# Kernel optimization log

Measured on AMD Instinct MI355X. Metric: run time of the kernel, lower is better.

Reference implementation:

```python
import jax, jax.numpy as jnp
import numpy as np

D = 1024      # model_dim
H = 2048      # expert hidden_dim
E = 8         # num routed experts
TOP_K = 2
N_SHARED = 1
B, S = 2, 1024


def setup_inputs() -> dict:
    key = jax.random.key(0)
    ks = jax.random.split(key, 12)
    sc = 0.02
    return {
        "hidden": jax.random.normal(ks[0], (B, S, D), jnp.float32),
        # router Linear(D -> E); stored as [in, out]
        "router_w": jax.random.normal(ks[1], (D, E), jnp.float32) * sc,
        "router_b": jnp.zeros((E,), jnp.float32),
        # shared expert (1): Linear(D->H), Linear(H->D)
        "sw1": jax.random.normal(ks[2], (D, H), jnp.float32) * sc,
        "sb1": jnp.zeros((H,), jnp.float32),
        "sw2": jax.random.normal(ks[3], (H, D), jnp.float32) * sc,
        "sb2": jnp.zeros((D,), jnp.float32),
        # routed experts, stacked over E
        "rw1": jax.random.normal(ks[4], (E, D, H), jnp.float32) * sc,
        "rb1": jnp.zeros((E, H), jnp.float32),
        "rw2": jax.random.normal(ks[5], (E, H, D), jnp.float32) * sc,
        "rb2": jnp.zeros((E, D), jnp.float32),
    }


def reference(hidden, router_w, router_b, sw1, sb1, sw2, sb2, rw1, rb1, rw2, rb2):
    b, s, d = hidden.shape
    T = b * s
    flat = hidden.reshape(T, d)                              # [T, D]

    # --- router ---
    router_logits = flat @ router_w + router_b               # [T, E]
    router_probs = jax.nn.softmax(router_logits, axis=-1)
    topk_probs, topk_idx = jax.lax.top_k(router_probs, TOP_K)  # [T, K]

    # per-(token, expert) mixing weight: sum of top-k probs that hit expert e
    weights = jnp.zeros_like(router_probs).at[
        jnp.arange(T)[:, None], topk_idx
    ].add(topk_probs)                                        # [T, E]

    # --- shared expert(s) (1 expert -> mean == itself) ---
    sh = jax.nn.gelu(flat @ sw1 + sb1, approximate=False)    # [T, H]
    shared_out = (sh @ sw2 + sb2) / N_SHARED                 # [T, D]

    # --- routed experts: dense all-expert eval weighted by routing weights ---
    # (identical math to the gather/FFN/index_add loop: weight is 0 for
    #  tokens not routed to expert e)
    h1 = jax.nn.gelu(jnp.einsum('td,edh->teh', flat, rw1) + rb1[None],
                     approximate=False)                      # [T, E, H]
    expert_out = jnp.einsum('teh,ehd->ted', h1, rw2) + rb2[None]  # [T, E, D]
    mixed = jnp.einsum('ted,te->td', expert_out, weights)    # [T, D]

    return (shared_out + mixed).reshape(b, s, d)
```

## Files before the change

### kernel.cpp

```cpp
#include <hip/hip_runtime.h>
#include <hip/hip_bf16.h>

#define T_TOK 2048
#define DDIM  1024
#define HDIM  2048
#define NEXP  8
#define NSEG  9

typedef unsigned short u16;
typedef __attribute__((ext_vector_type(4))) float f32x4;
typedef __attribute__((ext_vector_type(8))) short bf16x8;
typedef __attribute__((ext_vector_type(4))) unsigned short u16x4;

__device__ __forceinline__ u16 f2bf(float x) {
  union { float f; unsigned int u; } v; v.f = x;
  unsigned int r = v.u + 0x7fffu + ((v.u >> 16) & 1u);
  return (u16)(r >> 16);
}
__device__ __forceinline__ float gelu_exact(float x) {
  return 0.5f * x * (1.0f + erff(x * 0.70710678118654752f));
}

__device__ __forceinline__ void gload16(const void* g, void* l) {
  __builtin_amdgcn_global_load_lds(
      (const __attribute__((address_space(1))) unsigned int*)g,
      (__attribute__((address_space(3))) unsigned int*)l, 16, 0, 0);
}

__global__ __launch_bounds__(256) void router_kernel(
    const float* __restrict__ x, const float* __restrict__ rw,
    const float* __restrict__ rb, u16* __restrict__ xb,
    float* __restrict__ weights, int* __restrict__ counts,
    int* __restrict__ lists)
{
  int wv = threadIdx.x >> 6, lane = threadIdx.x & 63;
  int t = blockIdx.x * 4 + wv;
  const float* xrow = x + (size_t)t * DDIM;
  float acc[NEXP];
#pragma unroll
  for (int e = 0; e < NEXP; e++) acc[e] = 0.f;
#pragma unroll
  for (int i = 0; i < 4; i++) {
    int d0 = i * 256 + lane * 4;
    f32x4 xv = *(const f32x4*)(xrow + d0);
    u16x4 pk;
#pragma unroll
    for (int j = 0; j < 4; j++) {
      float xs = xv[j];
      pk[j] = f2bf(xs);
      const float* wr = rw + (size_t)(d0 + j) * NEXP;
#pragma unroll
      for (int e = 0; e < NEXP; e++) acc[e] = fmaf(xs, wr[e], acc[e]);
    }
    *(u16x4*)(xb + (size_t)t * DDIM + d0) = pk;
  }
#pragma unroll
  for (int off = 32; off >= 1; off >>= 1)
#pragma unroll
    for (int e = 0; e < NEXP; e++) acc[e] += __shfl_xor(acc[e], off);

  if (lane == 0) {
    float lg[NEXP], mx = -1e30f;
#pragma unroll
    for (int e = 0; e < NEXP; e++) { lg[e] = acc[e] + rb[e]; mx = fmaxf(mx, lg[e]); }
    float p[NEXP], s = 0.f;
#pragma unroll
    for (int e = 0; e < NEXP; e++) { p[e] = expf(lg[e] - mx); s += p[e]; }
    float inv = 1.0f / s;
#pragma unroll
    for (int e = 0; e < NEXP; e++) p[e] *= inv;
    int i1 = 0;
#pragma unroll
    for (int e = 1; e < NEXP; e++) if (p[e] > p[i1]) i1 = e;
    int i2 = (i1 == 0) ? 1 : 0;
#pragma unroll
    for (int e = 0; e < NEXP; e++) if (e != i1 && p[e] > p[i2]) i2 = e;
#pragma unroll
    for (int e = 0; e < NEXP; e++)
      weights[(size_t)t * NEXP + e] = (e == i1) ? p[i1] : (e == i2) ? p[i2] : 0.f;
    int p1 = atomicAdd(counts + i1, 1); lists[i1 * T_TOK + p1] = t;
    int p2 = atomicAdd(counts + i2, 1); lists[i2 * T_TOK + p2] = t;
    lists[NEXP * T_TOK + t] = t;
  }
}

__global__ void seg_kernel(int* counts, int* segoff, int* ytab, int* nyt) {
  counts[NEXP] = T_TOK;
  int off = 0, n = 0;
  for (int e = 0; e < NSEG; e++) {
    segoff[e] = off;
    int c = counts[e];
    for (int my = 0; my * 128 < c; my++) ytab[n++] = e * 256 + my;
    off += c;
  }
  *nyt = n;
}

__global__ __launch_bounds__(256) void transpose_bf16_kernel(
    const float* __restrict__ rin, const float* __restrict__ sin_,
    u16* __restrict__ rout, u16* __restrict__ sout, int R, int C)
{
  __shared__ float tile[32][33];
  int b = blockIdx.z;
  const float* inb = (b < NEXP) ? rin + (size_t)b * R * C : sin_;
  u16* outb = (b < NEXP) ? rout + (size_t)b * R * C : sout;
  int r0 = blockIdx.y * 32, c0 = blockIdx.x * 32;
  int tx = threadIdx.x & 31, ty = threadIdx.x >> 5;
#pragma unroll
  for (int j = 0; j < 4; j++) {
    int r = ty + j * 8;
    tile[r][tx] = inb[(size_t)(r0 + r) * C + c0 + tx];
  }
  __syncthreads();
#pragma unroll
  for (int j = 0; j < 4; j++) {
    int rr = ty + j * 8;
    outb[(size_t)(c0 + rr) * R + r0 + tx] = f2bf(tile[tx][rr]);
  }
}

__global__ __launch_bounds__(256) void gemm1_kernel(
    const u16* __restrict__ Xb, const u16* __restrict__ rw1t,
    const u16* __restrict__ sw1t, const float* __restrict__ rb1,
    const float* __restrict__ sb1, const int* __restrict__ counts,
    const int* __restrict__ segoff, const int* __restrict__ lists,
    const int* __restrict__ ytab, const int* __restrict__ nyt,
    u16* __restrict__ H1)
{
  __shared__ u16 Alds[128 * 64];
  __shared__ u16 Blds[128 * 64];

  int tid = threadIdx.x, wv = tid >> 6, lane = tid & 63;
  int wm = wv >> 1, wn = wv & 1;
  int col8 = (lane & 7) * 8;

  int ntile = nyt[0] * (HDIM / 128);
  for (int t = blockIdx.x; t < ntile; t += gridDim.x) {
    int yt = t >> 4, nx = t & 15;
    int em = ytab[yt];
    int e = em >> 8, m0 = (em & 255) * 128, n0 = nx * 128;
    int cnt = counts[e];
    const u16* Bt = (e < NEXP) ? (rw1t + (size_t)e * HDIM * DDIM) : sw1t;
    const float* bias = (e < NEXP) ? (rb1 + (size_t)e * HDIM) : sb1;
    const int* list = lists + e * T_TOK;
    int seg = segoff[e];

    size_t asrc[4], bsrc[4];
#pragma unroll
    for (int r = 0; r < 4; r++) {
      int srow = r * 32 + wv * 8 + (lane >> 3);
      int tok = list[min(m0 + srow, cnt - 1)];
      asrc[r] = (size_t)tok * DDIM + col8;
      bsrc[r] = (size_t)(n0 + srow) * DDIM + col8;
    }

    f32x4 acc[4][4];
#pragma unroll
    for (int i = 0; i < 4; i++)
#pragma unroll
      for (int j = 0; j < 4; j++) acc[i][j] = (f32x4){0.f, 0.f, 0.f, 0.f};

    for (int kk = 0; kk < DDIM; kk += 64) {
#pragma unroll
      for (int r = 0; r < 4; r++) {
        gload16(Xb + asrc[r] + kk, Alds + (size_t)(r * 256 + wv * 64 + lane) * 8);
        gload16(Bt + bsrc[r] + kk, Blds + (size_t)(r * 256 + wv * 64 + lane) * 8);
      }
      __syncthreads();
#pragma unroll
      for (int ks = 0; ks < 2; ks++) {
        int kb = ks * 32 + (lane >> 4) * 8;
        bf16x8 af[4], bfr[4];
#pragma unroll
        for (int f = 0; f < 4; f++) {
          af[f]  = *(const bf16x8*)(Alds + (wm * 64 + f * 16 + (lane & 15)) * 64 + kb);
          bfr[f] = *(const bf16x8*)(Blds + (wn * 64 + f * 16 + (lane & 15)) * 64 + kb);
        }
#pragma unroll
        for (int mf = 0; mf < 4; mf++)
#pragma unroll
          for (int nf = 0; nf < 4; nf++)
            acc[mf][nf] = __builtin_amdgcn_mfma_f32_16x16x32_bf16(af[mf], bfr[nf], acc[mf][nf], 0, 0, 0);
      }
      __syncthreads();
    }

#pragma unroll
    for (int nf = 0; nf < 4; nf++) {
      int col = n0 + wn * 64 + nf * 16 + (lane & 15);
      float b = bias[col];
#pragma unroll
      for (int mf = 0; mf < 4; mf++) {
#pragma unroll
        for (int rg = 0; rg < 4; rg++) {
          int mt = wm * 64 + mf * 16 + (lane >> 4) * 4 + rg;
          if (m0 + mt < cnt) {
            float v = acc[mf][nf][rg] + b;
            H1[(size_t)(seg + m0 + mt) * HDIM + col] = f2bf(gelu_exact(v));
          }
        }
      }
    }
  }
}

__global__ __launch_bounds__(256) void gemm2_kernel(
    const u16* __restrict__ H1, const u16* __restrict__ rw2t,
    const u16* __restrict__ sw2t, const float* __restrict__ rb2,
    const float* __restrict__ sb2, const float* __restrict__ weights,
    const int* __restrict__ counts, const int* __restrict__ segoff,
    const int* __restrict__ lists, const int* __restrict__ ytab,
    const int* __restrict__ nyt, float* __restrict__ out)
{
  __shared__ u16 Alds[128 * 64];
  __shared__ u16 Blds[128 * 64];

  int tid = threadIdx.x, wv = tid >> 6, lane = tid & 63;
  int wm = wv >> 1, wn = wv & 1;
  int col8 = (lane & 7) * 8;

  int ntile = nyt[0] * (DDIM / 128);
  for (int t = blockIdx.x; t < ntile; t += gridDim.x) {
    int yt = t >> 3, nx = t & 7;
    int em = ytab[yt];
    int e = em >> 8, m0 = (em & 255) * 128, n0 = nx * 128;
    int cnt = counts[e];
    const u16* Bt = (e < NEXP) ? (rw2t + (size_t)e * DDIM * HDIM) : sw2t;
    const float* bias = (e < NEXP) ? (rb2 + (size_t)e * DDIM) : sb2;
    const int* list = lists + e * T_TOK;
    int seg = segoff[e];

    size_t asrc[4], bsrc[4];
#pragma unroll
    for (int r = 0; r < 4; r++) {
      int srow = r * 32 + wv * 8 + (lane >> 3);
      asrc[r] = (size_t)(seg + min(m0 + srow, cnt - 1)) * HDIM + col8;
      bsrc[r] = (size_t)(n0 + srow) * HDIM + col8;
    }

    f32x4 acc[4][4];
#pragma unroll
    for (int i = 0; i < 4; i++)
#pragma unroll
      for (int j = 0; j < 4; j++) acc[i][j] = (f32x4){0.f, 0.f, 0.f, 0.f};

    for (int kk = 0; kk < HDIM; kk += 64) {
#pragma unroll
      for (int r = 0; r < 4; r++) {
        gload16(H1 + asrc[r] + kk, Alds + (size_t)(r * 256 + wv * 64 + lane) * 8);
        gload16(Bt + bsrc[r] + kk, Blds + (size_t)(r * 256 + wv * 64 + lane) * 8);
      }
      __syncthreads();
#pragma unroll
      for (int ks = 0; ks < 2; ks++) {
        int kb = ks * 32 + (lane >> 4) * 8;
        bf16x8 af[4], bfr[4];
#pragma unroll
        for (int f = 0; f < 4; f++) {
          af[f]  = *(const bf16x8*)(Alds + (wm * 64 + f * 16 + (lane & 15)) * 64 + kb);
          bfr[f] = *(const bf16x8*)(Blds + (wn * 64 + f * 16 + (lane & 15)) * 64 + kb);
        }
#pragma unroll
        for (int mf = 0; mf < 4; mf++)
#pragma unroll
          for (int nf = 0; nf < 4; nf++)
            acc[mf][nf] = __builtin_amdgcn_mfma_f32_16x16x32_bf16(af[mf], bfr[nf], acc[mf][nf], 0, 0, 0);
      }
      __syncthreads();
    }

    float biasv[4];
#pragma unroll
    for (int nf = 0; nf < 4; nf++) biasv[nf] = bias[n0 + wn * 64 + nf * 16 + (lane & 15)];

#pragma unroll
    for (int mf = 0; mf < 4; mf++) {
#pragma unroll
      for (int rg = 0; rg < 4; rg++) {
        int mt = wm * 64 + mf * 16 + (lane >> 4) * 4 + rg;
        int mrow = m0 + mt;
        if (mrow < cnt) {
          int tok = list[mrow];
          float w = (e < NEXP) ? weights[(size_t)tok * NEXP + e] : 1.0f;
          float* orow = out + (size_t)tok * DDIM + n0 + wn * 64 + (lane & 15);
#pragma unroll
          for (int nf = 0; nf < 4; nf++)
            atomicAdd(orow + nf * 16, w * (acc[mf][nf][rg] + biasv[nf]));
        }
      }
    }
  }
}

extern "C" void kernel_launch(void* const* d_in, const int* in_sizes, int n_in,
                              void* d_out, int out_size, void* d_ws, size_t ws_size,
                              hipStream_t stream) {
  (void)in_sizes; (void)n_in; (void)out_size; (void)ws_size;
  const float* hidden   = (const float*)d_in[0];
  const float* router_w = (const float*)d_in[1];
  const float* router_b = (const float*)d_in[2];
  const float* sw1 = (const float*)d_in[3];
  const float* sb1 = (const float*)d_in[4];
  const float* sw2 = (const float*)d_in[5];
  const float* sb2 = (const float*)d_in[6];
  const float* rw1 = (const float*)d_in[7];
  const float* rb1 = (const float*)d_in[8];
  const float* rw2 = (const float*)d_in[9];
  const float* rb2 = (const float*)d_in[10];
  float* out = (float*)d_out;

  char* ws = (char*)d_ws;
  u16* Xb      = (u16*)(ws + 0);
  u16* rw1t    = (u16*)(ws + 4194304);
  u16* rw2t    = (u16*)(ws + 37748736);
  u16* sw1t    = (u16*)(ws + 71303168);
  u16* sw2t    = (u16*)(ws + 75497472);
  u16* H1      = (u16*)(ws + 79691776);
  float* weights = (float*)(ws + 104857600);
  int* counts  = (int*)(ws + 104923136);
  int* segoff  = (int*)(ws + 104923200);
  int* lists   = (int*)(ws + 104923264);
  int* ytab    = (int*)(ws + 104996992);
  int* nyt     = (int*)(ws + 104997632);

  hipMemsetAsync(counts, 0, 64, stream);
  hipMemsetAsync(out, 0, (size_t)T_TOK * DDIM * sizeof(float), stream);

  router_kernel<<<T_TOK / 4, 256, 0, stream>>>(hidden, router_w, router_b, Xb,
                                               weights, counts, lists);
  seg_kernel<<<1, 1, 0, stream>>>(counts, segoff, ytab, nyt);

  transpose_bf16_kernel<<<dim3(HDIM / 32, DDIM / 32, NSEG), 256, 0, stream>>>(
      rw1, sw1, rw1t, sw1t, DDIM, HDIM);
  transpose_bf16_kernel<<<dim3(DDIM / 32, HDIM / 32, NSEG), 256, 0, stream>>>(
      rw2, sw2, rw2t, sw2t, HDIM, DDIM);

  gemm1_kernel<<<1024, 256, 0, stream>>>(
      Xb, rw1t, sw1t, rb1, sb1, counts, segoff, lists, ytab, nyt, H1);
  gemm2_kernel<<<1024, 256, 0, stream>>>(
      H1, rw2t, sw2t, rb2, sb2, weights, counts, segoff, lists, ytab, nyt, out);
}
```

Measured before the change: 256.1 us.

## Double-buffer LDS with XOR swizzle and split-K gemm2 into two halves

Both expert GEMMs now use a two-stage LDS ping-pong with K-step 32, so the global-to-LDS load of the next slice is issued before the MFMAs on the current slice. The LDS layout is XOR-swizzled to reduce bank conflicts on the fragment reads. gemm2 also splits K into two halves that run as separate tiles and combine through the existing atomicAdd, with bias added only by the first half. This doubles gemm2's tile count to fill the device better, at the cost of twice as many atomics on the output and halved MFMA work per barrier.

```diff
diff --git a/kernel.cpp b/kernel.cpp
--- a/kernel.cpp
+++ b/kernel.cpp
@@ -20,6 +20,7 @@
 __device__ __forceinline__ float gelu_exact(float x) {
   return 0.5f * x * (1.0f + erff(x * 0.70710678118654752f));
 }
+__device__ __forceinline__ int swz(int row) { return (row & 3) ^ ((row >> 2) & 3); }
 
 __device__ __forceinline__ void gload16(const void* g, void* l) {
   __builtin_amdgcn_global_load_lds(
@@ -127,12 +128,28 @@
     const int* __restrict__ ytab, const int* __restrict__ nyt,
     u16* __restrict__ H1)
 {
-  __shared__ u16 Alds[128 * 64];
-  __shared__ u16 Blds[128 * 64];
+  __shared__ u16 Alds[2][128 * 32];
+  __shared__ u16 Blds[2][128 * 32];
 
   int tid = threadIdx.x, wv = tid >> 6, lane = tid & 63;
   int wm = wv >> 1, wn = wv & 1;
-  int col8 = (lane & 7) * 8;
+
+  int srow[2], soff[2];
+#pragma unroll
+  for (int r = 0; r < 2; r++) {
+    int i = r * 256 + tid;
+    srow[r] = i >> 2;
+    soff[r] = ((i & 3) ^ swz(i >> 2)) * 8;
+  }
+  int kc = lane >> 4;
+  int aoff[4], boff[4];
+#pragma unroll
+  for (int f = 0; f < 4; f++) {
+    int ra = wm * 64 + f * 16 + (lane & 15);
+    int rb_ = wn * 64 + f * 16 + (lane & 15);
+    aoff[f] = ra * 32 + ((kc ^ swz(ra)) * 8);
+    boff[f] = rb_ * 32 + ((kc ^ swz(rb_)) * 8);
+  }
 
   int ntile = nyt[0] * (HDIM / 128);
   for (int t = blockIdx.x; t < ntile; t += gridDim.x) {
@@ -145,13 +162,12 @@
     const int* list = lists + e * T_TOK;
     int seg = segoff[e];
 
-    size_t asrc[4], bsrc[4];
-#pragma unroll
-    for (int r = 0; r < 4; r++) {
-      int srow = r * 32 + wv * 8 + (lane >> 3);
-      int tok = list[min(m0 + srow, cnt - 1)];
-      asrc[r] = (size_t)tok * DDIM + col8;
-      bsrc[r] = (size_t)(n0 + srow) * DDIM + col8;
+    size_t abase[2], bbase[2];
+#pragma unroll
+    for (int r = 0; r < 2; r++) {
+      int tok = list[min(m0 + srow[r], cnt - 1)];
+      abase[r] = (size_t)tok * DDIM + soff[r];
+      bbase[r] = (size_t)(n0 + srow[r]) * DDIM + soff[r];
     }
 
     f32x4 acc[4][4];
@@ -160,28 +176,37 @@
 #pragma unroll
       for (int j = 0; j < 4; j++) acc[i][j] = (f32x4){0.f, 0.f, 0.f, 0.f};
 
-    for (int kk = 0; kk < DDIM; kk += 64) {
-#pragma unroll
-      for (int r = 0; r < 4; r++) {
-        gload16(Xb + asrc[r] + kk, Alds + (size_t)(r * 256 + wv * 64 + lane) * 8);
-        gload16(Bt + bsrc[r] + kk, Blds + (size_t)(r * 256 + wv * 64 + lane) * 8);
-      }
-      __syncthreads();
-#pragma unroll
-      for (int ks = 0; ks < 2; ks++) {
-        int kb = ks * 32 + (lane >> 4) * 8;
-        bf16x8 af[4], bfr[4];
-#pragma unroll
-        for (int f = 0; f < 4; f++) {
-          af[f]  = *(const bf16x8*)(Alds + (wm * 64 + f * 16 + (lane & 15)) * 64 + kb);
-          bfr[f] = *(const bf16x8*)(Blds + (wn * 64 + f * 16 + (lane & 15)) * 64 + kb);
+#pragma unroll
+    for (int r = 0; r < 2; r++) {
+      int i = r * 256 + tid;
+      gload16(Xb + abase[r], &Alds[0][i * 8]);
+      gload16(Bt + bbase[r], &Blds[0][i * 8]);
+    }
+    __syncthreads();
+
+    const int NS = DDIM / 32;
+    for (int s = 0; s < NS; s++) {
+      int cur = s & 1;
+      if (s + 1 < NS) {
+        int kk = (s + 1) * 32;
+#pragma unroll
+        for (int r = 0; r < 2; r++) {
+          int i = r * 256 + tid;
+          gload16(Xb + abase[r] + kk, &Alds[cur ^ 1][i * 8]);
+          gload16(Bt + bbase[r] + kk, &Blds[cur ^ 1][i * 8]);
         }
-#pragma unroll
-        for (int mf = 0; mf < 4; mf++)
-#pragma unroll
-          for (int nf = 0; nf < 4; nf++)
-            acc[mf][nf] = __builtin_amdgcn_mfma_f32_16x16x32_bf16(af[mf], bfr[nf], acc[mf][nf], 0, 0, 0);
-      }
+      }
+      bf16x8 af[4], bfr[4];
+#pragma unroll
+      for (int f = 0; f < 4; f++) {
+        af[f]  = *(const bf16x8*)(&Alds[cur][aoff[f]]);
+        bfr[f] = *(const bf16x8*)(&Blds[cur][boff[f]]);
+      }
+#pragma unroll
+      for (int mf = 0; mf < 4; mf++)
+#pragma unroll
+        for (int nf = 0; nf < 4; nf++)
+          acc[mf][nf] = __builtin_amdgcn_mfma_f32_16x16x32_bf16(af[mf], bfr[nf], acc[mf][nf], 0, 0, 0);
       __syncthreads();
     }
 
@@ -201,6 +226,7 @@
         }
       }
     }
+    __syncthreads();
   }
 }
 
@@ -212,16 +238,32 @@
     const int* __restrict__ lists, const int* __restrict__ ytab,
     const int* __restrict__ nyt, float* __restrict__ out)
 {
-  __shared__ u16 Alds[128 * 64];
-  __shared__ u16 Blds[128 * 64];
+  __shared__ u16 Alds[2][128 * 32];
+  __shared__ u16 Blds[2][128 * 32];
 
   int tid = threadIdx.x, wv = tid >> 6, lane = tid & 63;
   int wm = wv >> 1, wn = wv & 1;
-  int col8 = (lane & 7) * 8;
-
-  int ntile = nyt[0] * (DDIM / 128);
+
+  int srow[2], soff[2];
+#pragma unroll
+  for (int r = 0; r < 2; r++) {
+    int i = r * 256 + tid;
+    srow[r] = i >> 2;
+    soff[r] = ((i & 3) ^ swz(i >> 2)) * 8;
+  }
+  int kc = lane >> 4;
+  int aoff[4], boff[4];
+#pragma unroll
+  for (int f = 0; f < 4; f++) {
+    int ra = wm * 64 + f * 16 + (lane & 15);
+    int rb_ = wn * 64 + f * 16 + (lane & 15);
+    aoff[f] = ra * 32 + ((kc ^ swz(ra)) * 8);
+    boff[f] = rb_ * 32 + ((kc ^ swz(rb_)) * 8);
+  }
+
+  int ntile = nyt[0] * (DDIM / 128) * 2;
   for (int t = blockIdx.x; t < ntile; t += gridDim.x) {
-    int yt = t >> 3, nx = t & 7;
+    int kh = t & 1, nx = (t >> 1) & 7, yt = t >> 4;
     int em = ytab[yt];
     int e = em >> 8, m0 = (em & 255) * 128, n0 = nx * 128;
     int cnt = counts[e];
@@ -229,13 +271,13 @@
     const float* bias = (e < NEXP) ? (rb2 + (size_t)e * DDIM) : sb2;
     const int* list = lists + e * T_TOK;
     int seg = segoff[e];
-
-    size_t asrc[4], bsrc[4];
-#pragma unroll
-    for (int r = 0; r < 4; r++) {
-      int srow = r * 32 + wv * 8 + (lane >> 3);
-      asrc[r] = (size_t)(seg + min(m0 + srow, cnt - 1)) * HDIM + col8;
-      bsrc[r] = (size_t)(n0 + srow) * HDIM + col8;
+    int k0 = kh * 1024;
+
+    size_t abase[2], bbase[2];
+#pragma unroll
+    for (int r = 0; r < 2; r++) {
+      abase[r] = (size_t)(seg + min(m0 + srow[r], cnt - 1)) * HDIM + k0 + soff[r];
+      bbase[r] = (size_t)(n0 + srow[r]) * HDIM + k0 + soff[r];
     }
 
     f32x4 acc[4][4];
@@ -244,34 +286,44 @@
 #pragma unroll
       for (int j = 0; j < 4; j++) acc[i][j] = (f32x4){0.f, 0.f, 0.f, 0.f};
 
-    for (int kk = 0; kk < HDIM; kk += 64) {
-#pragma unroll
-      for (int r = 0; r < 4; r++) {
-        gload16(H1 + asrc[r] + kk, Alds + (size_t)(r * 256 + wv * 64 + lane) * 8);
-        gload16(Bt + bsrc[r] + kk, Blds + (size_t)(r * 256 + wv * 64 + lane) * 8);
-      }
+#pragma unroll
+    for (int r = 0; r < 2; r++) {
+      int i = r * 256 + tid;
+      gload16(H1 + abase[r], &Alds[0][i * 8]);
+      gload16(Bt + bbase[r], &Blds[0][i * 8]);
+    }
+    __syncthreads();
+
+    const int NS = 1024 / 32;
+    for (int s = 0; s < NS; s++) {
+      int cur = s & 1;
+      if (s + 1 < NS) {
+        int kk = (s + 1) * 32;
+#pragma unroll
+        for (int r = 0; r < 2; r++) {
+          int i = r * 256 + tid;
+          gload16(H1 + abase[r] + kk, &Alds[cur ^ 1][i * 8]);
+          gload16(Bt + bbase[r] + kk, &Blds[cur ^ 1][i * 8]);
+        }
+      }
+      bf16x8 af[4], bfr[4];
+#pragma unroll
+      for (int f = 0; f < 4; f++) {
+        af[f]  = *(const bf16x8*)(&Alds[cur][aoff[f]]);
+        bfr[f] = *(const bf16x8*)(&Blds[cur][boff[f]]);
+      }
+#pragma unroll
+      for (int mf = 0; mf < 4; mf++)
+#pragma unroll
+        for (int nf = 0; nf < 4; nf++)
+          acc[mf][nf] = __builtin_amdgcn_mfma_f32_16x16x32_bf16(af[mf], bfr[nf], acc[mf][nf], 0, 0, 0);
       __syncthreads();
-#pragma unroll
-      for (int ks = 0; ks < 2; ks++) {
-        int kb = ks * 32 + (lane >> 4) * 8;
-        bf16x8 af[4], bfr[4];
-#pragma unroll
-        for (int f = 0; f < 4; f++) {
-          af[f]  = *(const bf16x8*)(Alds + (wm * 64 + f * 16 + (lane & 15)) * 64 + kb);
-          bfr[f] = *(const bf16x8*)(Blds + (wn * 64 + f * 16 + (lane & 15)) * 64 + kb);
-        }
-#pragma unroll
-        for (int mf = 0; mf < 4; mf++)
-#pragma unroll
-          for (int nf = 0; nf < 4; nf++)
-            acc[mf][nf] = __builtin_amdgcn_mfma_f32_16x16x32_bf16(af[mf], bfr[nf], acc[mf][nf], 0, 0, 0);
-      }
-      __syncthreads();
     }
 
     float biasv[4];
 #pragma unroll
-    for (int nf = 0; nf < 4; nf++) biasv[nf] = bias[n0 + wn * 64 + nf * 16 + (lane & 15)];
+    for (int nf = 0; nf < 4; nf++)
+      biasv[nf] = (kh == 0) ? bias[n0 + wn * 64 + nf * 16 + (lane & 15)] : 0.f;
 
 #pragma unroll
     for (int mf = 0; mf < 4; mf++) {
@@ -289,6 +341,7 @@
         }
       }
     }
+    __syncthreads();
   }
 }
 
```

Measured after the change: 283.5 us. +10.7%, slower.

## Fuse rw2 bf16 conversion into a pipelined, split-K, swizzled gemm2 kernel

Applied to the files above, without the earlier changes.

Drops the separate transpose/convert pass for the second-layer weights and has gemm2 read fp32 rw2/sw2 directly, converting them to bf16 in registers before storing into a swizzled LDS tile. The gemm2 kernel moves to 256x256 tiles on 512 threads, with a 4-stage async LDS ring for activations, a double-buffered B tile, split-K across two halves, and explicit waitcnt/setprio scheduling. This removes one full weight pass through memory, but it makes the GEMM read fp32 weights (twice the bytes) and doubles the atomic output traffic because of the split-K.

```diff
diff --git a/kernel.cpp b/kernel.cpp
--- a/kernel.cpp
+++ b/kernel.cpp
@@ -19,6 +19,9 @@
 }
 __device__ __forceinline__ float gelu_exact(float x) {
   return 0.5f * x * (1.0f + erff(x * 0.70710678118654752f));
+}
+__device__ __forceinline__ int swz4(int row) {
+  return (row & 3) ^ ((row >> 2) & 3);
 }
 
 __device__ __forceinline__ void gload16(const void* g, void* l) {
@@ -84,16 +87,19 @@
   }
 }
 
-__global__ void seg_kernel(int* counts, int* segoff, int* ytab, int* nyt) {
+__global__ void seg_kernel(int* counts, int* segoff, int* ytab1, int* nyt1,
+                           int* ytab2, int* nyt2) {
   counts[NEXP] = T_TOK;
-  int off = 0, n = 0;
+  int off = 0, n1 = 0, n2 = 0;
   for (int e = 0; e < NSEG; e++) {
     segoff[e] = off;
     int c = counts[e];
-    for (int my = 0; my * 128 < c; my++) ytab[n++] = e * 256 + my;
+    for (int my = 0; my * 128 < c; my++) ytab1[n1++] = e * 256 + my;
+    for (int my = 0; my * 256 < c; my++) ytab2[n2++] = e * 256 + my;
     off += c;
   }
-  *nyt = n;
+  *nyt1 = n1;
+  *nyt2 = n2;
 }
 
 __global__ __launch_bounds__(256) void transpose_bf16_kernel(
@@ -204,91 +210,158 @@
   }
 }
 
-__global__ __launch_bounds__(256) void gemm2_kernel(
-    const u16* __restrict__ H1, const u16* __restrict__ rw2t,
-    const u16* __restrict__ sw2t, const float* __restrict__ rb2,
+__global__ __launch_bounds__(512) void gemm2_kernel(
+    const u16* __restrict__ H1, const float* __restrict__ rw2,
+    const float* __restrict__ sw2, const float* __restrict__ rb2,
     const float* __restrict__ sb2, const float* __restrict__ weights,
     const int* __restrict__ counts, const int* __restrict__ segoff,
     const int* __restrict__ lists, const int* __restrict__ ytab,
     const int* __restrict__ nyt, float* __restrict__ out)
 {
-  __shared__ u16 Alds[128 * 64];
-  __shared__ u16 Blds[128 * 64];
-
-  int tid = threadIdx.x, wv = tid >> 6, lane = tid & 63;
-  int wm = wv >> 1, wn = wv & 1;
-  int col8 = (lane & 7) * 8;
-
-  int ntile = nyt[0] * (DDIM / 128);
+  __shared__ u16 Alds[4][256 * 32];
+  __shared__ u16 Blds[2][256 * 32];
+
+  int tid = threadIdx.x, lane = tid & 63;
+  int wv = tid >> 6, wm = wv >> 2, wn = wv & 3;
+  int kc = lane >> 4, lr = lane & 15;
+
+  int srow[2], soff[2];
+#pragma unroll
+  for (int j = 0; j < 2; j++) {
+    int i = j * 512 + tid;
+    srow[j] = i >> 2;
+    soff[j] = (((i & 3) ^ swz4(i >> 2)) * 8);
+  }
+  int aoff[8], boff[4];
+#pragma unroll
+  for (int f = 0; f < 8; f++) {
+    int ra = wm * 128 + f * 16 + lr;
+    aoff[f] = ra * 32 + ((kc ^ swz4(ra)) * 8);
+  }
+#pragma unroll
+  for (int f = 0; f < 4; f++) {
+    int rb_ = wn * 64 + f * 16 + lr;
+    boff[f] = rb_ * 32 + ((kc ^ swz4(rb_)) * 8);
+  }
+  int bw[4];
+#pragma unroll
+  for (int j = 0; j < 4; j++)
+    bw[j] = ((lane << 2) + j) * 32 + (((wv >> 1) ^ j ^ (lane & 3)) << 3) + ((wv & 1) << 2);
+
+  int ntile = nyt[0] * (DDIM / 256) * 2;
   for (int t = blockIdx.x; t < ntile; t += gridDim.x) {
-    int yt = t >> 3, nx = t & 7;
+    int kh = t & 1, nx = (t >> 1) & 3, yt = t >> 3;
     int em = ytab[yt];
-    int e = em >> 8, m0 = (em & 255) * 128, n0 = nx * 128;
+    int e = em >> 8, m0 = (em & 255) * 256, n0 = nx * 256;
     int cnt = counts[e];
-    const u16* Bt = (e < NEXP) ? (rw2t + (size_t)e * DDIM * HDIM) : sw2t;
+    const float* Wf = (e < NEXP) ? (rw2 + (size_t)e * HDIM * DDIM) : sw2;
     const float* bias = (e < NEXP) ? (rb2 + (size_t)e * DDIM) : sb2;
     const int* list = lists + e * T_TOK;
     int seg = segoff[e];
-
-    size_t asrc[4], bsrc[4];
-#pragma unroll
-    for (int r = 0; r < 4; r++) {
-      int srow = r * 32 + wv * 8 + (lane >> 3);
-      asrc[r] = (size_t)(seg + min(m0 + srow, cnt - 1)) * HDIM + col8;
-      bsrc[r] = (size_t)(n0 + srow) * HDIM + col8;
-    }
-
-    f32x4 acc[4][4];
-#pragma unroll
-    for (int i = 0; i < 4; i++)
+    int k0 = kh * 1024;
+
+    size_t abase[2];
+#pragma unroll
+    for (int j = 0; j < 2; j++)
+      abase[j] = (size_t)(seg + min(m0 + srow[j], cnt - 1)) * HDIM + k0 + soff[j];
+    const float* Wb = Wf + (size_t)k0 * DDIM + n0 + (lane << 2);
+
+    f32x4 acc[8][4];
+#pragma unroll
+    for (int i = 0; i < 8; i++)
 #pragma unroll
       for (int j = 0; j < 4; j++) acc[i][j] = (f32x4){0.f, 0.f, 0.f, 0.f};
 
-    for (int kk = 0; kk < HDIM; kk += 64) {
-#pragma unroll
-      for (int r = 0; r < 4; r++) {
-        gload16(H1 + asrc[r] + kk, Alds + (size_t)(r * 256 + wv * 64 + lane) * 8);
-        gload16(Bt + bsrc[r] + kk, Blds + (size_t)(r * 256 + wv * 64 + lane) * 8);
-      }
-      __syncthreads();
-#pragma unroll
-      for (int ks = 0; ks < 2; ks++) {
-        int kb = ks * 32 + (lane >> 4) * 8;
-        bf16x8 af[4], bfr[4];
-#pragma unroll
-        for (int f = 0; f < 4; f++) {
-          af[f]  = *(const bf16x8*)(Alds + (wm * 64 + f * 16 + (lane & 15)) * 64 + kb);
-          bfr[f] = *(const bf16x8*)(Blds + (wn * 64 + f * 16 + (lane & 15)) * 64 + kb);
+    const int NS = 1024 / 32;
+    f32x4 vBa, vBb, vBc, vBd;
+    {
+      const float* Wk = Wb + (size_t)(wv * 4) * DDIM;
+      vBa = *(const f32x4*)(Wk);
+      vBb = *(const f32x4*)(Wk + DDIM);
+      vBc = *(const f32x4*)(Wk + 2 * DDIM);
+      vBd = *(const f32x4*)(Wk + 3 * DDIM);
+    }
+#pragma unroll
+    for (int s = 0; s < 2; s++)
+#pragma unroll
+      for (int j = 0; j < 2; j++) {
+        int i = j * 512 + tid;
+        gload16(H1 + abase[j] + s * 32, &Alds[s][i * 8]);
+      }
+
+    for (int s = 0; s < NS; s++) {
+      if (s + 2 < NS) {
+        int kk = (s + 2) * 32;
+        int nb = (s + 2) & 3;
+#pragma unroll
+        for (int j = 0; j < 2; j++) {
+          int i = j * 512 + tid;
+          gload16(H1 + abase[j] + kk, &Alds[nb][i * 8]);
         }
-#pragma unroll
-        for (int mf = 0; mf < 4; mf++)
-#pragma unroll
-          for (int nf = 0; nf < 4; nf++)
-            acc[mf][nf] = __builtin_amdgcn_mfma_f32_16x16x32_bf16(af[mf], bfr[nf], acc[mf][nf], 0, 0, 0);
-      }
-      __syncthreads();
+      }
+      {
+        u16* Bd = &Blds[s & 1][0];
+#pragma unroll
+        for (int j = 0; j < 4; j++) {
+          u16x4 pk;
+          pk[0] = f2bf(vBa[j]); pk[1] = f2bf(vBb[j]);
+          pk[2] = f2bf(vBc[j]); pk[3] = f2bf(vBd[j]);
+          *(u16x4*)(Bd + bw[j]) = pk;
+        }
+      }
+      if (s + 1 < NS) {
+        const float* Wk = Wb + (size_t)((s + 1) * 32 + wv * 4) * DDIM;
+        vBa = *(const f32x4*)(Wk);
+        vBb = *(const f32x4*)(Wk + DDIM);
+        vBc = *(const f32x4*)(Wk + 2 * DDIM);
+        vBd = *(const f32x4*)(Wk + 3 * DDIM);
+      }
+      if (s + 2 < NS)      asm volatile("s_waitcnt vmcnt(8)" ::: "memory");
+      else if (s + 1 < NS) asm volatile("s_waitcnt vmcnt(6)" ::: "memory");
+      else                 asm volatile("s_waitcnt vmcnt(0)" ::: "memory");
+      asm volatile("s_waitcnt lgkmcnt(0)" ::: "memory");
+      __builtin_amdgcn_s_barrier();
+      __builtin_amdgcn_sched_barrier(0);
+
+      const u16* Ac = &Alds[s & 3][0];
+      const u16* Bc = &Blds[s & 1][0];
+      bf16x8 af[8], bfr[4];
+#pragma unroll
+      for (int f = 0; f < 8; f++) af[f] = *(const bf16x8*)(Ac + aoff[f]);
+#pragma unroll
+      for (int f = 0; f < 4; f++) bfr[f] = *(const bf16x8*)(Bc + boff[f]);
+      __builtin_amdgcn_s_setprio(1);
+#pragma unroll
+      for (int mf = 0; mf < 8; mf++)
+#pragma unroll
+        for (int nf = 0; nf < 4; nf++)
+          acc[mf][nf] = __builtin_amdgcn_mfma_f32_16x16x32_bf16(af[mf], bfr[nf], acc[mf][nf], 0, 0, 0);
+      __builtin_amdgcn_s_setprio(0);
     }
 
     float biasv[4];
 #pragma unroll
-    for (int nf = 0; nf < 4; nf++) biasv[nf] = bias[n0 + wn * 64 + nf * 16 + (lane & 15)];
-
-#pragma unroll
-    for (int mf = 0; mf < 4; mf++) {
+    for (int nf = 0; nf < 4; nf++)
+      biasv[nf] = (kh == 0) ? bias[n0 + wn * 64 + nf * 16 + lr] : 0.f;
+
+#pragma unroll
+    for (int mf = 0; mf < 8; mf++) {
 #pragma unroll
       for (int rg = 0; rg < 4; rg++) {
-        int mt = wm * 64 + mf * 16 + (lane >> 4) * 4 + rg;
+        int mt = wm * 128 + mf * 16 + kc * 4 + rg;
         int mrow = m0 + mt;
         if (mrow < cnt) {
           int tok = list[mrow];
           float w = (e < NEXP) ? weights[(size_t)tok * NEXP + e] : 1.0f;
-          float* orow = out + (size_t)tok * DDIM + n0 + wn * 64 + (lane & 15);
+          float* orow = out + (size_t)tok * DDIM + n0 + wn * 64 + lr;
 #pragma unroll
           for (int nf = 0; nf < 4; nf++)
             atomicAdd(orow + nf * 16, w * (acc[mf][nf][rg] + biasv[nf]));
         }
       }
     }
+    __builtin_amdgcn_s_barrier();
+    __builtin_amdgcn_sched_barrier(0);
   }
 }
 
@@ -312,31 +385,29 @@
   char* ws = (char*)d_ws;
   u16* Xb      = (u16*)(ws + 0);
   u16* rw1t    = (u16*)(ws + 4194304);
-  u16* rw2t    = (u16*)(ws + 37748736);
-  u16* sw1t    = (u16*)(ws + 71303168);
-  u16* sw2t    = (u16*)(ws + 75497472);
-  u16* H1      = (u16*)(ws + 79691776);
-  float* weights = (float*)(ws + 104857600);
-  int* counts  = (int*)(ws + 104923136);
-  int* segoff  = (int*)(ws + 104923200);
-  int* lists   = (int*)(ws + 104923264);
-  int* ytab    = (int*)(ws + 104996992);
-  int* nyt     = (int*)(ws + 104997632);
+  u16* sw1t    = (u16*)(ws + 37748736);
+  u16* H1      = (u16*)(ws + 41943040);
+  float* weights = (float*)(ws + 67108864);
+  int* counts  = (int*)(ws + 67174400);
+  int* segoff  = (int*)(ws + 67174464);
+  int* lists   = (int*)(ws + 67174528);
+  int* ytab1   = (int*)(ws + 67248256);
+  int* nyt1    = (int*)(ws + 67248896);
+  int* ytab2   = (int*)(ws + 67248960);
+  int* nyt2    = (int*)(ws + 67249600);
 
   hipMemsetAsync(counts, 0, 64, stream);
   hipMemsetAsync(out, 0, (size_t)T_TOK * DDIM * sizeof(float), stream);
 
   router_kernel<<<T_TOK / 4, 256, 0, stream>>>(hidden, router_w, router_b, Xb,
                                                weights, counts, lists);
-  seg_kernel<<<1, 1, 0, stream>>>(counts, segoff, ytab, nyt);
+  seg_kernel<<<1, 1, 0, stream>>>(counts, segoff, ytab1, nyt1, ytab2, nyt2);
 
   transpose_bf16_kernel<<<dim3(HDIM / 32, DDIM / 32, NSEG), 256, 0, stream>>>(
       rw1, sw1, rw1t, sw1t, DDIM, HDIM);
-  transpose_bf16_kernel<<<dim3(DDIM / 32, HDIM / 32, NSEG), 256, 0, stream>>>(
-      rw2, sw2, rw2t, sw2t, HDIM, DDIM);
 
   gemm1_kernel<<<1024, 256, 0, stream>>>(
-      Xb, rw1t, sw1t, rb1, sb1, counts, segoff, lists, ytab, nyt, H1);
-  gemm2_kernel<<<1024, 256, 0, stream>>>(
-      H1, rw2t, sw2t, rb2, sb2, weights, counts, segoff, lists, ytab, nyt, out);
-}
+      Xb, rw1t, sw1t, rb1, sb1, counts, segoff, lists, ytab1, nyt1, H1);
+  gemm2_kernel<<<256, 512, 0, stream>>>(
+      H1, rw2, sw2, rb2, sb2, weights, counts, segoff, lists, ytab2, nyt2, out);
+}
```

Result: faster. 245.7 us (-4.1%).
